# Performance work log

Hardware: AMD Instinct MI355X
Metric: run time of the kernel (lower is better)

## Reference

```python
import jax, jax.numpy as jnp
import numpy as np

B, N, D, H, DH, E, BIAS_DIM = 8, 512, 512, 8, 64, 32768, 8

def setup_inputs() -> dict:
    key = jax.random.key(0)
    ks = jax.random.split(key, 10)
    states = jax.random.normal(ks[0], (B, N, D), jnp.float32)
    key_states = jax.random.normal(ks[1], (B, N, D), jnp.float32)
    # causal mask, broadcastable over heads: [B,1,N,N]
    masks = jnp.broadcast_to(jnp.tril(jnp.ones((N, N), jnp.float32)), (B, 1, N, N))
    edge_type = jax.random.randint(ks[2], (E, 1), 0, BIAS_DIM, jnp.int32)
    b_idx = jax.random.randint(ks[3], (E, 1), 0, B, jnp.int32)
    q_idx = jax.random.randint(ks[4], (E, 1), 0, N, jnp.int32)
    k_idx = jax.random.randint(ks[5], (E, 1), 0, N, jnp.int32)
    attention_bias = jnp.concatenate([edge_type, b_idx, q_idx, k_idx], axis=1)
    s = 0.05
    Wq = jax.random.normal(ks[6], (D, H, DH), jnp.float32) * s
    Wk = jax.random.normal(ks[7], (D, H, DH), jnp.float32) * s
    Wv = jax.random.normal(ks[8], (D, H, DH), jnp.float32) * s
    k2 = jax.random.split(ks[9], 3)
    Wo = jax.random.normal(k2[0], (H, DH, D), jnp.float32) * s
    bias_embs = jax.random.normal(k2[1], (BIAS_DIM, DH), jnp.float32) * s
    bias_scalar = jax.random.normal(k2[2], (DH, 1), jnp.float32) * s
    return {"states": states, "key_states": key_states, "masks": masks,
            "attention_bias": attention_bias, "Wq": Wq, "Wk": Wk, "Wv": Wv,
            "Wo": Wo, "bias_embs": bias_embs, "bias_scalar": bias_scalar}

def reference(states, key_states, masks, attention_bias, Wq, Wk, Wv, Wo, bias_embs, bias_scalar):
    q = jnp.einsum('btd,dha->btha', states, Wq)
    k = jnp.einsum('btd,dha->btha', key_states, Wk)
    v = jnp.einsum('btd,dha->btha', key_states, Wv)
    alpha = jnp.einsum('bkha,bqha->bhqk', k, q)  # [B,H,Q,K]
    # sparse edge bias: embed edge types, project to scalar, scatter into [B,Q,K]
    et = attention_bias[:, 0]
    bias_vals = (bias_embs[et] @ bias_scalar)[:, 0]  # [E]
    bq, bk = alpha.shape[2], alpha.shape[3]
    bias_mat = jnp.zeros((alpha.shape[0], bq, bk), alpha.dtype)
    bias_mat = bias_mat.at[attention_bias[:, 1], attention_bias[:, 2], attention_bias[:, 3]].add(bias_vals)
    summed_keys = jnp.sum(k, axis=-1)  # [B,K,H]
    alpha = alpha + jnp.einsum('bqk,bkh->bhqk', bias_mat, summed_keys)
    alpha = alpha * jax.lax.rsqrt(jnp.float32(DH))
    neg = jnp.finfo(jnp.float32).min
    alpha = alpha * masks + (1.0 - jnp.ceil(masks)) * neg
    alpha = jax.nn.softmax(alpha, axis=-1)
    alpha = alpha * masks
    context = jnp.einsum('bhqk,bkha->bqha', alpha, v)
    return jnp.einsum('btha,had->btd', context, Wo)
```

## Files before the change

kernel.cpp:

```cpp
#include <hip/hip_runtime.h>

typedef unsigned short u16;
typedef unsigned int u32;
typedef __bf16 bf16x8 __attribute__((ext_vector_type(8)));
typedef float f32x4 __attribute__((ext_vector_type(4)));
typedef u16 u16x8 __attribute__((ext_vector_type(8)));
typedef u16 u16x4 __attribute__((ext_vector_type(4)));


__device__ __forceinline__ u16 f2b(float f) {
  union { float f; u32 i; } v; v.f = f;
  u32 r = v.i + 0x7fffu + ((v.i >> 16) & 1u);
  return (u16)(r >> 16);
}
__device__ __forceinline__ float b2f(u16 u) {
  union { u32 i; float f; } v; v.i = ((u32)u) << 16; return v.f;
}

__global__ void cvt_bf16(const float* __restrict__ s0, const float* __restrict__ s1,
                         u16* __restrict__ d0, u16* __restrict__ d1) {
  const float* src = blockIdx.y ? s1 : s0;
  u16* dst = blockIdx.y ? d1 : d0;
  int gid = blockIdx.x * 256 + threadIdx.x;
  const float4* sp = (const float4*)src + (size_t)gid * 2;
  float4 x0 = sp[0], x1 = sp[1];
  u16x8 p;
  p[0] = f2b(x0.x); p[1] = f2b(x0.y); p[2] = f2b(x0.z); p[3] = f2b(x0.w);
  p[4] = f2b(x1.x); p[5] = f2b(x1.y); p[6] = f2b(x1.z); p[7] = f2b(x1.w);
  *(u16x8*)(dst + (size_t)gid * 8) = p;
}

__global__ void transpose_w(const float* __restrict__ w0, const float* __restrict__ w1,
                            const float* __restrict__ w2, const float* __restrict__ w3,
                            u16* __restrict__ o0, u16* __restrict__ o1,
                            u16* __restrict__ o2, u16* __restrict__ o3) {
  __shared__ u16 t[32][33];
  const float* src; u16* dst; float sc = 1.f;
  if (blockIdx.z == 0)      { src = w0; dst = o0; sc = 0.125f; }
  else if (blockIdx.z == 1) { src = w1; dst = o1; }
  else if (blockIdx.z == 2) { src = w2; dst = o2; }
  else                      { src = w3; dst = o3; }
  int tx = threadIdx.x, ty = threadIdx.y;
  int c0 = blockIdx.x * 32, r0 = blockIdx.y * 32;
  #pragma unroll
  for (int i = ty; i < 32; i += 8) t[i][tx] = f2b(src[(r0 + i) * 512 + c0 + tx] * sc);
  __syncthreads();
  #pragma unroll
  for (int i = ty; i < 32; i += 8) dst[(c0 + i) * 512 + r0 + tx] = t[tx][i];
}

__global__ void scatter_bias(const int* __restrict__ ab, const float* __restrict__ be,
                             const float* __restrict__ bsc, float* __restrict__ bias_mat,
                             int n_edges) {
  __shared__ float tv[8];
  int tid = threadIdx.x;
  if (tid < 8) {
    float s = 0.f;
    #pragma unroll
    for (int a = 0; a < 64; a++) s += be[tid * 64 + a] * bsc[a];
    tv[tid] = s * 0.125f;
  }
  __syncthreads();
  int e = blockIdx.x * 256 + tid;
  if (e < n_edges) {
    int et = ab[e * 4 + 0];
    int b  = ab[e * 4 + 1];
    int qi = ab[e * 4 + 2];
    int ki = ab[e * 4 + 3];
    atomicAdd(&bias_mat[((size_t)b * 512 + qi) * 512 + ki], tv[et]);
  }
}

__global__ __launch_bounds__(256) void qkv_gemm(const u16* __restrict__ sb,
                                                const u16* __restrict__ kbin,
                                                const u16* __restrict__ wT,
                                                u16* __restrict__ qb,
                                                u16* __restrict__ kbo,
                                                u16* __restrict__ vtb) {
  __shared__ u16 As[128 * 72];
  __shared__ u16 Bs[128 * 72];
  int tid = threadIdx.x;
  int lane = tid & 63, wave = tid >> 6;
  int quad = lane >> 4, ln = lane & 15;
  int wr = wave >> 1, wc = wave & 1;
  int row0 = blockIdx.x * 128;
  int col0 = blockIdx.y * 128;
  const u16* A = (col0 < 512) ? sb : kbin;
  int ar = tid >> 1;
  int ac = (tid & 1) * 32;

  f32x4 acc[4][4];
  #pragma unroll
  for (int i = 0; i < 4; i++)
    #pragma unroll
    for (int j = 0; j < 4; j++) acc[i][j] = (f32x4){0.f, 0.f, 0.f, 0.f};

  const u16* ap = A + (size_t)(row0 + ar) * 512 + ac;
  const u16* bp = wT + (size_t)(col0 + ar) * 512 + ac;

  u16x8 ra0, ra1, ra2, ra3, rb0, rb1, rb2, rb3;
  ra0 = *(const u16x8*)(ap + 0);  ra1 = *(const u16x8*)(ap + 8);
  ra2 = *(const u16x8*)(ap + 16); ra3 = *(const u16x8*)(ap + 24);
  rb0 = *(const u16x8*)(bp + 0);  rb1 = *(const u16x8*)(bp + 8);
  rb2 = *(const u16x8*)(bp + 16); rb3 = *(const u16x8*)(bp + 24);

  for (int k0 = 0; k0 < 512; k0 += 64) {
    __syncthreads();
    *(u16x8*)&As[ar * 72 + ac + 0]  = ra0;  *(u16x8*)&As[ar * 72 + ac + 8]  = ra1;
    *(u16x8*)&As[ar * 72 + ac + 16] = ra2;  *(u16x8*)&As[ar * 72 + ac + 24] = ra3;
    *(u16x8*)&Bs[ar * 72 + ac + 0]  = rb0;  *(u16x8*)&Bs[ar * 72 + ac + 8]  = rb1;
    *(u16x8*)&Bs[ar * 72 + ac + 16] = rb2;  *(u16x8*)&Bs[ar * 72 + ac + 24] = rb3;
    __syncthreads();
    if (k0 < 448) {
      int kn = k0 + 64;
      ra0 = *(const u16x8*)(ap + kn + 0);  ra1 = *(const u16x8*)(ap + kn + 8);
      ra2 = *(const u16x8*)(ap + kn + 16); ra3 = *(const u16x8*)(ap + kn + 24);
      rb0 = *(const u16x8*)(bp + kn + 0);  rb1 = *(const u16x8*)(bp + kn + 8);
      rb2 = *(const u16x8*)(bp + kn + 16); rb3 = *(const u16x8*)(bp + kn + 24);
    }
    #pragma unroll
    for (int s = 0; s < 2; s++) {
      bf16x8 af[4], bfv[4];
      #pragma unroll
      for (int i = 0; i < 4; i++)
        af[i] = *(bf16x8*)&As[(wr * 64 + i * 16 + ln) * 72 + s * 32 + quad * 8];
      #pragma unroll
      for (int j = 0; j < 4; j++)
        bfv[j] = *(bf16x8*)&Bs[(wc * 64 + j * 16 + ln) * 72 + s * 32 + quad * 8];
      #pragma unroll
      for (int i = 0; i < 4; i++)
        #pragma unroll
        for (int j = 0; j < 4; j++)
          acc[i][j] = __builtin_amdgcn_mfma_f32_16x16x32_bf16(af[i], bfv[j], acc[i][j], 0, 0, 0);
    }
  }

  int region = col0 >> 9;
  int nbase = col0 & 511;
  if (region <= 1) {
    u16* Cout = region ? kbo : qb;
    #pragma unroll
    for (int i = 0; i < 4; i++)
      #pragma unroll
      for (int j = 0; j < 4; j++) {
        int mb = row0 + wr * 64 + i * 16 + quad * 4;
        int n = nbase + wc * 64 + j * 16 + ln;
        #pragma unroll
        for (int r = 0; r < 4; r++)
          Cout[(size_t)(mb + r) * 512 + n] = f2b(acc[i][j][r]);
      }
  } else {
    #pragma unroll
    for (int i = 0; i < 4; i++)
      #pragma unroll
      for (int j = 0; j < 4; j++) {
        int mb = row0 + wr * 64 + i * 16 + quad * 4;
        int bb = mb >> 9, t0 = mb & 511;
        int a_abs = nbase + wc * 64 + j * 16 + ln;
        int h = a_abs >> 6, a = a_abs & 63;
        u16x4 p;
        p[0] = f2b(acc[i][j][0]); p[1] = f2b(acc[i][j][1]);
        p[2] = f2b(acc[i][j][2]); p[3] = f2b(acc[i][j][3]);
        *(u16x4*)&vtb[(((size_t)bb * 8 + h) * 64 + a) * 512 + t0] = p;
      }
  }
}

__global__ __launch_bounds__(256) void out_gemm(const u16* __restrict__ A,
                                                const u16* __restrict__ BT,
                                                float* __restrict__ C) {
  __shared__ u16 As[128 * 72];
  __shared__ u16 Bs[128 * 72];
  int tid = threadIdx.x;
  int lane = tid & 63, wave = tid >> 6;
  int quad = lane >> 4, ln = lane & 15;
  int wr = wave >> 1, wc = wave & 1;
  int row0 = blockIdx.x * 128;
  int col0 = blockIdx.y * 128;
  int ar = tid >> 1;
  int ac = (tid & 1) * 32;

  f32x4 acc[4][4];
  #pragma unroll
  for (int i = 0; i < 4; i++)
    #pragma unroll
    for (int j = 0; j < 4; j++) acc[i][j] = (f32x4){0.f, 0.f, 0.f, 0.f};

  const u16* ap = A + (size_t)(row0 + ar) * 512 + ac;
  const u16* bp = BT + (size_t)(col0 + ar) * 512 + ac;

  u16x8 ra0, ra1, ra2, ra3, rb0, rb1, rb2, rb3;
  ra0 = *(const u16x8*)(ap + 0);  ra1 = *(const u16x8*)(ap + 8);
  ra2 = *(const u16x8*)(ap + 16); ra3 = *(const u16x8*)(ap + 24);
  rb0 = *(const u16x8*)(bp + 0);  rb1 = *(const u16x8*)(bp + 8);
  rb2 = *(const u16x8*)(bp + 16); rb3 = *(const u16x8*)(bp + 24);

  for (int k0 = 0; k0 < 512; k0 += 64) {
    __syncthreads();
    *(u16x8*)&As[ar * 72 + ac + 0]  = ra0;  *(u16x8*)&As[ar * 72 + ac + 8]  = ra1;
    *(u16x8*)&As[ar * 72 + ac + 16] = ra2;  *(u16x8*)&As[ar * 72 + ac + 24] = ra3;
    *(u16x8*)&Bs[ar * 72 + ac + 0]  = rb0;  *(u16x8*)&Bs[ar * 72 + ac + 8]  = rb1;
    *(u16x8*)&Bs[ar * 72 + ac + 16] = rb2;  *(u16x8*)&Bs[ar * 72 + ac + 24] = rb3;
    __syncthreads();
    if (k0 < 448) {
      int kn = k0 + 64;
      ra0 = *(const u16x8*)(ap + kn + 0);  ra1 = *(const u16x8*)(ap + kn + 8);
      ra2 = *(const u16x8*)(ap + kn + 16); ra3 = *(const u16x8*)(ap + kn + 24);
      rb0 = *(const u16x8*)(bp + kn + 0);  rb1 = *(const u16x8*)(bp + kn + 8);
      rb2 = *(const u16x8*)(bp + kn + 16); rb3 = *(const u16x8*)(bp + kn + 24);
    }
    #pragma unroll
    for (int s = 0; s < 2; s++) {
      bf16x8 af[4], bfv[4];
      #pragma unroll
      for (int i = 0; i < 4; i++)
        af[i] = *(bf16x8*)&As[(wr * 64 + i * 16 + ln) * 72 + s * 32 + quad * 8];
      #pragma unroll
      for (int j = 0; j < 4; j++)
        bfv[j] = *(bf16x8*)&Bs[(wc * 64 + j * 16 + ln) * 72 + s * 32 + quad * 8];
      #pragma unroll
      for (int i = 0; i < 4; i++)
        #pragma unroll
        for (int j = 0; j < 4; j++)
          acc[i][j] = __builtin_amdgcn_mfma_f32_16x16x32_bf16(af[i], bfv[j], acc[i][j], 0, 0, 0);
    }
  }
  #pragma unroll
  for (int i = 0; i < 4; i++)
    #pragma unroll
    for (int j = 0; j < 4; j++) {
      int mb = row0 + wr * 64 + i * 16 + quad * 4;
      int n = col0 + wc * 64 + j * 16 + ln;
      #pragma unroll
      for (int r = 0; r < 4; r++)
        C[(size_t)(mb + r) * 512 + n] = acc[i][j][r];
    }
}

__global__ void sumk2(const u16* __restrict__ k, float* __restrict__ summed) {
  int tri = blockIdx.x * 4 + (threadIdx.x >> 6);
  int lane = threadIdx.x & 63;
  int bh = tri >> 9, t = tri & 511;
  int b = bh >> 3, h = bh & 7;
  float x = b2f(k[((size_t)(b * 512 + t)) * 512 + h * 64 + lane]);
  #pragma unroll
  for (int o = 32; o; o >>= 1) x += __shfl_xor(x, o);
  if (lane == 0) summed[tri] = x;
}

__global__ __launch_bounds__(256) void attn_mfma(const u16* __restrict__ q,
                                                 const u16* __restrict__ k,
                                                 const u16* __restrict__ vt,
                                                 const float* __restrict__ bias_mat,
                                                 const float* __restrict__ summed,
                                                 u16* __restrict__ ctx) {
  __shared__ u16 Qs[64 * 72];
  __shared__ u16 Ks[64 * 72];
  __shared__ u16 Vt[64 * 72];
  __shared__ u16 Ps[4][16 * 72];
  int tid = threadIdx.x;
  int wave = tid >> 6, lane = tid & 63;
  int quad = lane >> 4, ln = lane & 15;
  int blk = blockIdx.x;
  int qt = blk & 7, bh = blk >> 3;
  int b = bh >> 3, h = bh & 7;
  int q0 = qt * 64;

  int sr = tid >> 2;
  int sc2 = (tid & 3) * 16;

  {
    const u16* qp = q + ((size_t)(b * 512 + q0 + sr)) * 512 + h * 64 + sc2;
    *(u16x8*)&Qs[sr * 72 + sc2] = *(const u16x8*)qp;
    *(u16x8*)&Qs[sr * 72 + sc2 + 8] = *(const u16x8*)(qp + 8);
  }

  float m_r[4], l_r[4];
  f32x4 o[4];
  #pragma unroll
  for (int r = 0; r < 4; r++) { m_r[r] = -3.40282347e38f; l_r[r] = 0.f; }
  #pragma unroll
  for (int nt = 0; nt < 4; nt++) o[nt] = (f32x4){0.f, 0.f, 0.f, 0.f};

  int last = qt;
  const u16* kp0 = k + ((size_t)(b * 512 + sr)) * 512 + h * 64 + sc2;
  const u16* vp0 = vt + ((size_t)(bh * 64 + sr)) * 512 + sc2;

  u16x8 rk0 = *(const u16x8*)kp0;
  u16x8 rk1 = *(const u16x8*)(kp0 + 8);
  u16x8 rv0 = *(const u16x8*)vp0;
  u16x8 rv1 = *(const u16x8*)(vp0 + 8);

  for (int kb = 0; kb <= last; kb++) {
    __syncthreads();
    *(u16x8*)&Ks[sr * 72 + sc2] = rk0;
    *(u16x8*)&Ks[sr * 72 + sc2 + 8] = rk1;
    *(u16x8*)&Vt[sr * 72 + sc2] = rv0;
    *(u16x8*)&Vt[sr * 72 + sc2 + 8] = rv1;
    __syncthreads();
    if (kb < last) {
      const u16* kp = kp0 + (size_t)(kb + 1) * 64 * 512;
      const u16* vp = vp0 + (kb + 1) * 64;
      rk0 = *(const u16x8*)kp;
      rk1 = *(const u16x8*)(kp + 8);
      rv0 = *(const u16x8*)vp;
      rv1 = *(const u16x8*)(vp + 8);
    }

    int qrow = q0 + wave * 16 + quad * 4;
    float skv[4], bias_r[4][4];
    #pragma unroll
    for (int nt = 0; nt < 4; nt++) {
      int t = kb * 64 + nt * 16 + ln;
      skv[nt] = summed[bh * 512 + t];
      const float* bp = bias_mat + ((size_t)(b * 512 + qrow)) * 512 + t;
      #pragma unroll
      for (int r = 0; r < 4; r++) bias_r[nt][r] = bp[(size_t)r * 512];
    }

    bf16x8 aq0 = *(bf16x8*)&Qs[(wave * 16 + ln) * 72 + quad * 8];
    bf16x8 aq1 = *(bf16x8*)&Qs[(wave * 16 + ln) * 72 + 32 + quad * 8];
    f32x4 s[4];
    #pragma unroll
    for (int nt = 0; nt < 4; nt++) {
      bf16x8 b0 = *(bf16x8*)&Ks[(nt * 16 + ln) * 72 + quad * 8];
      bf16x8 b1 = *(bf16x8*)&Ks[(nt * 16 + ln) * 72 + 32 + quad * 8];
      s[nt] = (f32x4){0.f, 0.f, 0.f, 0.f};
      s[nt] = __builtin_amdgcn_mfma_f32_16x16x32_bf16(aq0, b0, s[nt], 0, 0, 0);
      s[nt] = __builtin_amdgcn_mfma_f32_16x16x32_bf16(aq1, b1, s[nt], 0, 0, 0);
    }

    #pragma unroll
    for (int nt = 0; nt < 4; nt++) {
      int t = kb * 64 + nt * 16 + ln;
      #pragma unroll
      for (int r = 0; r < 4; r++) {
        float val = s[nt][r] + bias_r[nt][r] * skv[nt];
        s[nt][r] = (t <= qrow + r) ? val : -3.40282347e38f;
      }
    }

    float alpha[4];
    #pragma unroll
    for (int r = 0; r < 4; r++) {
      float tm = fmaxf(fmaxf(s[0][r], s[1][r]), fmaxf(s[2][r], s[3][r]));
      #pragma unroll
      for (int off = 8; off; off >>= 1) tm = fmaxf(tm, __shfl_xor(tm, off));
      float mn = fmaxf(m_r[r], tm);
      alpha[r] = __expf(m_r[r] - mn);
      m_r[r] = mn;
      float rs = 0.f;
      #pragma unroll
      for (int nt = 0; nt < 4; nt++) {
        float p = __expf(s[nt][r] - mn);
        s[nt][r] = p;
        rs += p;
      }
      #pragma unroll
      for (int off = 8; off; off >>= 1) rs += __shfl_xor(rs, off);
      l_r[r] = l_r[r] * alpha[r] + rs;
    }

    #pragma unroll
    for (int nt = 0; nt < 4; nt++)
      #pragma unroll
      for (int r = 0; r < 4; r++)
        Ps[wave][(quad * 4 + r) * 72 + nt * 16 + ln] = f2b(s[nt][r]);
    #pragma unroll
    for (int nt = 0; nt < 4; nt++)
      #pragma unroll
      for (int r = 0; r < 4; r++)
        o[nt][r] *= alpha[r];

    bf16x8 ap0 = *(bf16x8*)&Ps[wave][ln * 72 + quad * 8];
    bf16x8 ap1 = *(bf16x8*)&Ps[wave][ln * 72 + 32 + quad * 8];
    #pragma unroll
    for (int nt = 0; nt < 4; nt++) {
      bf16x8 b0 = *(bf16x8*)&Vt[(nt * 16 + ln) * 72 + quad * 8];
      bf16x8 b1 = *(bf16x8*)&Vt[(nt * 16 + ln) * 72 + 32 + quad * 8];
      o[nt] = __builtin_amdgcn_mfma_f32_16x16x32_bf16(ap0, b0, o[nt], 0, 0, 0);
      o[nt] = __builtin_amdgcn_mfma_f32_16x16x32_bf16(ap1, b1, o[nt], 0, 0, 0);
    }
  }

  #pragma unroll
  for (int r = 0; r < 4; r++) {
    float inv = 1.f / l_r[r];
    int qrow = q0 + wave * 16 + quad * 4 + r;
    u16* dst = ctx + ((size_t)(b * 512 + qrow)) * 512 + h * 64;
    #pragma unroll
    for (int nt = 0; nt < 4; nt++)
      dst[nt * 16 + ln] = f2b(o[nt][r] * inv);
  }
}

extern "C" void kernel_launch(void* const* d_in, const int* in_sizes, int n_in,
                              void* d_out, int out_size, void* d_ws, size_t ws_size,
                              hipStream_t stream) {
  const float* states     = (const float*)d_in[0];
  const float* key_states = (const float*)d_in[1];
  const int*   ab         = (const int*)d_in[3];
  const float* Wq         = (const float*)d_in[4];
  const float* Wk         = (const float*)d_in[5];
  const float* Wv         = (const float*)d_in[6];
  const float* Wo         = (const float*)d_in[7];
  const float* be         = (const float*)d_in[8];
  const float* bsc        = (const float*)d_in[9];
  float* out = (float*)d_out;

  char* ws = (char*)d_ws;
  const size_t MB = 1024 * 1024;
  u16* wqt      = (u16*)(ws);
  u16* wkt      = (u16*)(ws + 512 * 1024);
  u16* wvt      = (u16*)(ws + 1024 * 1024);
  u16* wot      = (u16*)(ws + 1536 * 1024);
  u16* sb       = (u16*)(ws + 2 * MB);
  u16* kbin     = (u16*)(ws + 6 * MB);
  u16* qb       = (u16*)(ws + 10 * MB);
  u16* kbo      = (u16*)(ws + 14 * MB);
  u16* vtb      = (u16*)(ws + 18 * MB);
  u16* ctxb     = (u16*)(ws + 22 * MB);
  float* bias_m = (float*)(ws + 26 * MB);
  float* summed = (float*)(ws + 34 * MB);

  int n_edges = in_sizes[3] / 4;

  hipMemsetAsync(bias_m, 0, (size_t)8 * MB, stream);
  cvt_bf16<<<dim3(1024, 2), 256, 0, stream>>>(states, key_states, sb, kbin);
  transpose_w<<<dim3(16, 16, 4), dim3(32, 8), 0, stream>>>(Wq, Wk, Wv, Wo, wqt, wkt, wvt, wot);
  scatter_bias<<<dim3((n_edges + 255) / 256), 256, 0, stream>>>(ab, be, bsc, bias_m, n_edges);
  qkv_gemm<<<dim3(32, 12), 256, 0, stream>>>(sb, kbin, wqt, qb, kbo, vtb);
  sumk2<<<dim3(8192), 256, 0, stream>>>(kbo, summed);
  attn_mfma<<<dim3(512), 256, 0, stream>>>(qb, kbo, vtb, bias_m, summed, ctxb);
  out_gemm<<<dim3(32, 4), 256, 0, stream>>>(ctxb, wot, out);
}
```

Measured before the change: 156.6 us.

## Fuse prologue kernels, vectorize key sum, and pair causal query tiles per block

Merges the bf16 conversion, weight transpose and bias scatter into one prologue launch. The key-sum kernel now has each thread load eight bf16 values and reduce over eight lanes, which cuts its grid from 8192 blocks to 1024. Each attention block now handles two query tiles (p and 7-p), so every block does the same amount of causal work, and the grid drops from 512 to 256 blocks. The intent is to cut launch overhead and the tail imbalance of causal attention, at the cost of fewer attention blocks in flight and serial work within each block.

```diff
diff --git a/kernel.cpp b/kernel.cpp
--- a/kernel.cpp
+++ b/kernel.cpp
@@ -17,57 +17,61 @@
   union { u32 i; float f; } v; v.i = ((u32)u) << 16; return v.f;
 }
 
-__global__ void cvt_bf16(const float* __restrict__ s0, const float* __restrict__ s1,
-                         u16* __restrict__ d0, u16* __restrict__ d1) {
-  const float* src = blockIdx.y ? s1 : s0;
-  u16* dst = blockIdx.y ? d1 : d0;
-  int gid = blockIdx.x * 256 + threadIdx.x;
-  const float4* sp = (const float4*)src + (size_t)gid * 2;
-  float4 x0 = sp[0], x1 = sp[1];
-  u16x8 p;
-  p[0] = f2b(x0.x); p[1] = f2b(x0.y); p[2] = f2b(x0.z); p[3] = f2b(x0.w);
-  p[4] = f2b(x1.x); p[5] = f2b(x1.y); p[6] = f2b(x1.z); p[7] = f2b(x1.w);
-  *(u16x8*)(dst + (size_t)gid * 8) = p;
-}
-
-__global__ void transpose_w(const float* __restrict__ w0, const float* __restrict__ w1,
-                            const float* __restrict__ w2, const float* __restrict__ w3,
-                            u16* __restrict__ o0, u16* __restrict__ o1,
-                            u16* __restrict__ o2, u16* __restrict__ o3) {
+__global__ __launch_bounds__(256) void prologue(
+    const float* __restrict__ states, const float* __restrict__ key_states,
+    const float* __restrict__ Wq, const float* __restrict__ Wk,
+    const float* __restrict__ Wv, const float* __restrict__ Wo,
+    const int* __restrict__ ab, const float* __restrict__ be,
+    const float* __restrict__ bsc,
+    u16* __restrict__ sb, u16* __restrict__ kbin, u16* __restrict__ wbase,
+    float* __restrict__ bias_mat, int n_edges) {
   __shared__ u16 t[32][33];
-  const float* src; u16* dst; float sc = 1.f;
-  if (blockIdx.z == 0)      { src = w0; dst = o0; sc = 0.125f; }
-  else if (blockIdx.z == 1) { src = w1; dst = o1; }
-  else if (blockIdx.z == 2) { src = w2; dst = o2; }
-  else                      { src = w3; dst = o3; }
-  int tx = threadIdx.x, ty = threadIdx.y;
-  int c0 = blockIdx.x * 32, r0 = blockIdx.y * 32;
-  #pragma unroll
-  for (int i = ty; i < 32; i += 8) t[i][tx] = f2b(src[(r0 + i) * 512 + c0 + tx] * sc);
-  __syncthreads();
-  #pragma unroll
-  for (int i = ty; i < 32; i += 8) dst[(c0 + i) * 512 + r0 + tx] = t[tx][i];
-}
-
-__global__ void scatter_bias(const int* __restrict__ ab, const float* __restrict__ be,
-                             const float* __restrict__ bsc, float* __restrict__ bias_mat,
-                             int n_edges) {
   __shared__ float tv[8];
+  int bid = blockIdx.x;
   int tid = threadIdx.x;
-  if (tid < 8) {
-    float s = 0.f;
-    #pragma unroll
-    for (int a = 0; a < 64; a++) s += be[tid * 64 + a] * bsc[a];
-    tv[tid] = s * 0.125f;
-  }
-  __syncthreads();
-  int e = blockIdx.x * 256 + tid;
-  if (e < n_edges) {
-    int et = ab[e * 4 + 0];
-    int b  = ab[e * 4 + 1];
-    int qi = ab[e * 4 + 2];
-    int ki = ab[e * 4 + 3];
-    atomicAdd(&bias_mat[((size_t)b * 512 + qi) * 512 + ki], tv[et]);
+  if (bid < 2048) {
+    const float* src = (bid >= 1024) ? key_states : states;
+    u16* dst = (bid >= 1024) ? kbin : sb;
+    int gid = (bid & 1023) * 256 + tid;
+    const float4* sp = (const float4*)src + (size_t)gid * 2;
+    float4 x0 = sp[0], x1 = sp[1];
+    u16x8 p;
+    p[0] = f2b(x0.x); p[1] = f2b(x0.y); p[2] = f2b(x0.z); p[3] = f2b(x0.w);
+    p[4] = f2b(x1.x); p[5] = f2b(x1.y); p[6] = f2b(x1.z); p[7] = f2b(x1.w);
+    *(u16x8*)(dst + (size_t)gid * 8) = p;
+  } else if (bid < 3072) {
+    int tt = bid - 2048;
+    int z = tt >> 8, rem = tt & 255;
+    int bx = rem & 15, by = rem >> 4;
+    const float* src; float sc = 1.f;
+    if (z == 0)      { src = Wq; sc = 0.125f; }
+    else if (z == 1) { src = Wk; }
+    else if (z == 2) { src = Wv; }
+    else             { src = Wo; }
+    u16* dst = wbase + (size_t)z * 262144;
+    int tx = tid & 31, ty = tid >> 5;
+    int c0 = bx * 32, r0 = by * 32;
+    #pragma unroll
+    for (int i = ty; i < 32; i += 8) t[i][tx] = f2b(src[(r0 + i) * 512 + c0 + tx] * sc);
+    __syncthreads();
+    #pragma unroll
+    for (int i = ty; i < 32; i += 8) dst[(c0 + i) * 512 + r0 + tx] = t[tx][i];
+  } else {
+    if (tid < 8) {
+      float s = 0.f;
+      #pragma unroll
+      for (int a = 0; a < 64; a++) s += be[tid * 64 + a] * bsc[a];
+      tv[tid] = s * 0.125f;
+    }
+    __syncthreads();
+    int e = (bid - 3072) * 256 + tid;
+    if (e < n_edges) {
+      int et = ab[e * 4 + 0];
+      int b  = ab[e * 4 + 1];
+      int qi = ab[e * 4 + 2];
+      int ki = ab[e * 4 + 3];
+      atomicAdd(&bias_mat[((size_t)b * 512 + qi) * 512 + ki], tv[et]);
+    }
   }
 }
 
@@ -237,15 +241,21 @@
     }
 }
 
-__global__ void sumk2(const u16* __restrict__ k, float* __restrict__ summed) {
-  int tri = blockIdx.x * 4 + (threadIdx.x >> 6);
-  int lane = threadIdx.x & 63;
-  int bh = tri >> 9, t = tri & 511;
-  int b = bh >> 3, h = bh & 7;
-  float x = b2f(k[((size_t)(b * 512 + t)) * 512 + h * 64 + lane]);
+__global__ __launch_bounds__(256) void sumk2(const u16* __restrict__ k,
+                                             float* __restrict__ summed) {
+  int gid = blockIdx.x * 256 + threadIdx.x;
+  int group = gid >> 3;
+  int b = group >> 12, rem = group & 4095;
+  int t = rem >> 3, h = rem & 7;
+  int j = gid & 7;
+  u16x8 x = *(const u16x8*)(k + ((size_t)(b * 512 + t)) * 512 + h * 64 + j * 8);
+  float s = 0.f;
   #pragma unroll
-  for (int o = 32; o; o >>= 1) x += __shfl_xor(x, o);
-  if (lane == 0) summed[tri] = x;
+  for (int e = 0; e < 8; e++) s += b2f(x[e]);
+  s += __shfl_xor(s, 1);
+  s += __shfl_xor(s, 2);
+  s += __shfl_xor(s, 4);
+  if (j == 0) summed[(b * 8 + h) * 512 + t] = s;
 }
 
 __global__ __launch_bounds__(256) void attn_mfma(const u16* __restrict__ q,
@@ -262,135 +272,140 @@
   int wave = tid >> 6, lane = tid & 63;
   int quad = lane >> 4, ln = lane & 15;
   int blk = blockIdx.x;
-  int qt = blk & 7, bh = blk >> 3;
+  int p = blk & 3, bh = blk >> 2;
   int b = bh >> 3, h = bh & 7;
-  int q0 = qt * 64;
 
   int sr = tid >> 2;
   int sc2 = (tid & 3) * 16;
 
-  {
-    const u16* qp = q + ((size_t)(b * 512 + q0 + sr)) * 512 + h * 64 + sc2;
-    *(u16x8*)&Qs[sr * 72 + sc2] = *(const u16x8*)qp;
-    *(u16x8*)&Qs[sr * 72 + sc2 + 8] = *(const u16x8*)(qp + 8);
-  }
-
-  float m_r[4], l_r[4];
-  f32x4 o[4];
-  #pragma unroll
-  for (int r = 0; r < 4; r++) { m_r[r] = -3.40282347e38f; l_r[r] = 0.f; }
-  #pragma unroll
-  for (int nt = 0; nt < 4; nt++) o[nt] = (f32x4){0.f, 0.f, 0.f, 0.f};
-
-  int last = qt;
   const u16* kp0 = k + ((size_t)(b * 512 + sr)) * 512 + h * 64 + sc2;
   const u16* vp0 = vt + ((size_t)(bh * 64 + sr)) * 512 + sc2;
 
-  u16x8 rk0 = *(const u16x8*)kp0;
-  u16x8 rk1 = *(const u16x8*)(kp0 + 8);
-  u16x8 rv0 = *(const u16x8*)vp0;
-  u16x8 rv1 = *(const u16x8*)(vp0 + 8);
-
-  for (int kb = 0; kb <= last; kb++) {
-    __syncthreads();
-    *(u16x8*)&Ks[sr * 72 + sc2] = rk0;
-    *(u16x8*)&Ks[sr * 72 + sc2 + 8] = rk1;
-    *(u16x8*)&Vt[sr * 72 + sc2] = rv0;
-    *(u16x8*)&Vt[sr * 72 + sc2 + 8] = rv1;
-    __syncthreads();
-    if (kb < last) {
-      const u16* kp = kp0 + (size_t)(kb + 1) * 64 * 512;
-      const u16* vp = vp0 + (kb + 1) * 64;
-      rk0 = *(const u16x8*)kp;
-      rk1 = *(const u16x8*)(kp + 8);
-      rv0 = *(const u16x8*)vp;
-      rv1 = *(const u16x8*)(vp + 8);
-    }
-
-    int qrow = q0 + wave * 16 + quad * 4;
-    float skv[4], bias_r[4][4];
-    #pragma unroll
-    for (int nt = 0; nt < 4; nt++) {
-      int t = kb * 64 + nt * 16 + ln;
-      skv[nt] = summed[bh * 512 + t];
-      const float* bp = bias_mat + ((size_t)(b * 512 + qrow)) * 512 + t;
-      #pragma unroll
-      for (int r = 0; r < 4; r++) bias_r[nt][r] = bp[(size_t)r * 512];
-    }
-
-    bf16x8 aq0 = *(bf16x8*)&Qs[(wave * 16 + ln) * 72 + quad * 8];
-    bf16x8 aq1 = *(bf16x8*)&Qs[(wave * 16 + ln) * 72 + 32 + quad * 8];
-    f32x4 s[4];
-    #pragma unroll
-    for (int nt = 0; nt < 4; nt++) {
-      bf16x8 b0 = *(bf16x8*)&Ks[(nt * 16 + ln) * 72 + quad * 8];
-      bf16x8 b1 = *(bf16x8*)&Ks[(nt * 16 + ln) * 72 + 32 + quad * 8];
-      s[nt] = (f32x4){0.f, 0.f, 0.f, 0.f};
-      s[nt] = __builtin_amdgcn_mfma_f32_16x16x32_bf16(aq0, b0, s[nt], 0, 0, 0);
-      s[nt] = __builtin_amdgcn_mfma_f32_16x16x32_bf16(aq1, b1, s[nt], 0, 0, 0);
-    }
-
-    #pragma unroll
-    for (int nt = 0; nt < 4; nt++) {
-      int t = kb * 64 + nt * 16 + ln;
+  #pragma unroll
+  for (int ph = 0; ph < 2; ph++) {
+    int qt = ph ? (7 - p) : p;
+    int q0 = qt * 64;
+
+    __syncthreads();
+    {
+      const u16* qp = q + ((size_t)(b * 512 + q0 + sr)) * 512 + h * 64 + sc2;
+      *(u16x8*)&Qs[sr * 72 + sc2] = *(const u16x8*)qp;
+      *(u16x8*)&Qs[sr * 72 + sc2 + 8] = *(const u16x8*)(qp + 8);
+    }
+
+    float m_r[4], l_r[4];
+    f32x4 o[4];
+    #pragma unroll
+    for (int r = 0; r < 4; r++) { m_r[r] = -3.40282347e38f; l_r[r] = 0.f; }
+    #pragma unroll
+    for (int nt = 0; nt < 4; nt++) o[nt] = (f32x4){0.f, 0.f, 0.f, 0.f};
+
+    u16x8 rk0 = *(const u16x8*)kp0;
+    u16x8 rk1 = *(const u16x8*)(kp0 + 8);
+    u16x8 rv0 = *(const u16x8*)vp0;
+    u16x8 rv1 = *(const u16x8*)(vp0 + 8);
+
+    for (int kb = 0; kb <= qt; kb++) {
+      __syncthreads();
+      *(u16x8*)&Ks[sr * 72 + sc2] = rk0;
+      *(u16x8*)&Ks[sr * 72 + sc2 + 8] = rk1;
+      *(u16x8*)&Vt[sr * 72 + sc2] = rv0;
+      *(u16x8*)&Vt[sr * 72 + sc2 + 8] = rv1;
+      __syncthreads();
+      if (kb < qt) {
+        const u16* kp = kp0 + (size_t)(kb + 1) * 64 * 512;
+        const u16* vp = vp0 + (kb + 1) * 64;
+        rk0 = *(const u16x8*)kp;
+        rk1 = *(const u16x8*)(kp + 8);
+        rv0 = *(const u16x8*)vp;
+        rv1 = *(const u16x8*)(vp + 8);
+      }
+
+      int qrow = q0 + wave * 16 + quad * 4;
+      float skv[4], bias_r[4][4];
+      #pragma unroll
+      for (int nt = 0; nt < 4; nt++) {
+        int t = kb * 64 + nt * 16 + ln;
+        skv[nt] = summed[bh * 512 + t];
+        const float* bp = bias_mat + ((size_t)(b * 512 + qrow)) * 512 + t;
+        #pragma unroll
+        for (int r = 0; r < 4; r++) bias_r[nt][r] = bp[(size_t)r * 512];
+      }
+
+      bf16x8 aq0 = *(bf16x8*)&Qs[(wave * 16 + ln) * 72 + quad * 8];
+      bf16x8 aq1 = *(bf16x8*)&Qs[(wave * 16 + ln) * 72 + 32 + quad * 8];
+      f32x4 s[4];
+      #pragma unroll
+      for (int nt = 0; nt < 4; nt++) {
+        bf16x8 b0 = *(bf16x8*)&Ks[(nt * 16 + ln) * 72 + quad * 8];
+        bf16x8 b1 = *(bf16x8*)&Ks[(nt * 16 + ln) * 72 + 32 + quad * 8];
+        s[nt] = (f32x4){0.f, 0.f, 0.f, 0.f};
+        s[nt] = __builtin_amdgcn_mfma_f32_16x16x32_bf16(aq0, b0, s[nt], 0, 0, 0);
+        s[nt] = __builtin_amdgcn_mfma_f32_16x16x32_bf16(aq1, b1, s[nt], 0, 0, 0);
+      }
+
+      #pragma unroll
+      for (int nt = 0; nt < 4; nt++) {
+        int t = kb * 64 + nt * 16 + ln;
+        #pragma unroll
+        for (int r = 0; r < 4; r++) {
+          float val = s[nt][r] + bias_r[nt][r] * skv[nt];
+          s[nt][r] = (t <= qrow + r) ? val : -3.40282347e38f;
+        }
+      }
+
+      float alpha[4];
       #pragma unroll
       for (int r = 0; r < 4; r++) {
-        float val = s[nt][r] + bias_r[nt][r] * skv[nt];
-        s[nt][r] = (t <= qrow + r) ? val : -3.40282347e38f;
-      }
-    }
-
-    float alpha[4];
+        float tm = fmaxf(fmaxf(s[0][r], s[1][r]), fmaxf(s[2][r], s[3][r]));
+        #pragma unroll
+        for (int off = 8; off; off >>= 1) tm = fmaxf(tm, __shfl_xor(tm, off));
+        float mn = fmaxf(m_r[r], tm);
+        alpha[r] = __expf(m_r[r] - mn);
+        m_r[r] = mn;
+        float rs = 0.f;
+        #pragma unroll
+        for (int nt = 0; nt < 4; nt++) {
+          float pp = __expf(s[nt][r] - mn);
+          s[nt][r] = pp;
+          rs += pp;
+        }
+        #pragma unroll
+        for (int off = 8; off; off >>= 1) rs += __shfl_xor(rs, off);
+        l_r[r] = l_r[r] * alpha[r] + rs;
+      }
+
+      #pragma unroll
+      for (int nt = 0; nt < 4; nt++)
+        #pragma unroll
+        for (int r = 0; r < 4; r++)
+          Ps[wave][(quad * 4 + r) * 72 + nt * 16 + ln] = f2b(s[nt][r]);
+      #pragma unroll
+      for (int nt = 0; nt < 4; nt++)
+        #pragma unroll
+        for (int r = 0; r < 4; r++)
+          o[nt][r] *= alpha[r];
+
+      bf16x8 ap0 = *(bf16x8*)&Ps[wave][ln * 72 + quad * 8];
+      bf16x8 ap1 = *(bf16x8*)&Ps[wave][ln * 72 + 32 + quad * 8];
+      #pragma unroll
+      for (int nt = 0; nt < 4; nt++) {
+        bf16x8 b0 = *(bf16x8*)&Vt[(nt * 16 + ln) * 72 + quad * 8];
+        bf16x8 b1 = *(bf16x8*)&Vt[(nt * 16 + ln) * 72 + 32 + quad * 8];
+        o[nt] = __builtin_amdgcn_mfma_f32_16x16x32_bf16(ap0, b0, o[nt], 0, 0, 0);
+        o[nt] = __builtin_amdgcn_mfma_f32_16x16x32_bf16(ap1, b1, o[nt], 0, 0, 0);
+      }
+    }
+
     #pragma unroll
     for (int r = 0; r < 4; r++) {
-      float tm = fmaxf(fmaxf(s[0][r], s[1][r]), fmaxf(s[2][r], s[3][r]));
-      #pragma unroll
-      for (int off = 8; off; off >>= 1) tm = fmaxf(tm, __shfl_xor(tm, off));
-      float mn = fmaxf(m_r[r], tm);
-      alpha[r] = __expf(m_r[r] - mn);
-      m_r[r] = mn;
-      float rs = 0.f;
-      #pragma unroll
-      for (int nt = 0; nt < 4; nt++) {
-        float p = __expf(s[nt][r] - mn);
-        s[nt][r] = p;
-        rs += p;
-      }
-      #pragma unroll
-      for (int off = 8; off; off >>= 1) rs += __shfl_xor(rs, off);
-      l_r[r] = l_r[r] * alpha[r] + rs;
-    }
-
-    #pragma unroll
-    for (int nt = 0; nt < 4; nt++)
-      #pragma unroll
-      for (int r = 0; r < 4; r++)
-        Ps[wave][(quad * 4 + r) * 72 + nt * 16 + ln] = f2b(s[nt][r]);
-    #pragma unroll
-    for (int nt = 0; nt < 4; nt++)
-      #pragma unroll
-      for (int r = 0; r < 4; r++)
-        o[nt][r] *= alpha[r];
-
-    bf16x8 ap0 = *(bf16x8*)&Ps[wave][ln * 72 + quad * 8];
-    bf16x8 ap1 = *(bf16x8*)&Ps[wave][ln * 72 + 32 + quad * 8];
-    #pragma unroll
-    for (int nt = 0; nt < 4; nt++) {
-      bf16x8 b0 = *(bf16x8*)&Vt[(nt * 16 + ln) * 72 + quad * 8];
-      bf16x8 b1 = *(bf16x8*)&Vt[(nt * 16 + ln) * 72 + 32 + quad * 8];
-      o[nt] = __builtin_amdgcn_mfma_f32_16x16x32_bf16(ap0, b0, o[nt], 0, 0, 0);
-      o[nt] = __builtin_amdgcn_mfma_f32_16x16x32_bf16(ap1, b1, o[nt], 0, 0, 0);
-    }
-  }
-
-  #pragma unroll
-  for (int r = 0; r < 4; r++) {
-    float inv = 1.f / l_r[r];
-    int qrow = q0 + wave * 16 + quad * 4 + r;
-    u16* dst = ctx + ((size_t)(b * 512 + qrow)) * 512 + h * 64;
-    #pragma unroll
-    for (int nt = 0; nt < 4; nt++)
-      dst[nt * 16 + ln] = f2b(o[nt][r] * inv);
+      float inv = 1.f / l_r[r];
+      int qrow = q0 + wave * 16 + quad * 4 + r;
+      u16* dst = ctx + ((size_t)(b * 512 + qrow)) * 512 + h * 64;
+      #pragma unroll
+      for (int nt = 0; nt < 4; nt++)
+        dst[nt * 16 + ln] = f2b(o[nt][r] * inv);
+    }
   }
 }
 
@@ -410,9 +425,7 @@
 
   char* ws = (char*)d_ws;
   const size_t MB = 1024 * 1024;
-  u16* wqt      = (u16*)(ws);
-  u16* wkt      = (u16*)(ws + 512 * 1024);
-  u16* wvt      = (u16*)(ws + 1024 * 1024);
+  u16* wbase    = (u16*)(ws);
   u16* wot      = (u16*)(ws + 1536 * 1024);
   u16* sb       = (u16*)(ws + 2 * MB);
   u16* kbin     = (u16*)(ws + 6 * MB);
@@ -426,11 +439,10 @@
   int n_edges = in_sizes[3] / 4;
 
   hipMemsetAsync(bias_m, 0, (size_t)8 * MB, stream);
-  cvt_bf16<<<dim3(1024, 2), 256, 0, stream>>>(states, key_states, sb, kbin);
-  transpose_w<<<dim3(16, 16, 4), dim3(32, 8), 0, stream>>>(Wq, Wk, Wv, Wo, wqt, wkt, wvt, wot);
-  scatter_bias<<<dim3((n_edges + 255) / 256), 256, 0, stream>>>(ab, be, bsc, bias_m, n_edges);
-  qkv_gemm<<<dim3(32, 12), 256, 0, stream>>>(sb, kbin, wqt, qb, kbo, vtb);
-  sumk2<<<dim3(8192), 256, 0, stream>>>(kbo, summed);
-  attn_mfma<<<dim3(512), 256, 0, stream>>>(qb, kbo, vtb, bias_m, summed, ctxb);
+  prologue<<<dim3(3072 + (n_edges + 255) / 256), 256, 0, stream>>>(
+      states, key_states, Wq, Wk, Wv, Wo, ab, be, bsc, sb, kbin, wbase, bias_m, n_edges);
+  qkv_gemm<<<dim3(32, 12), 256, 0, stream>>>(sb, kbin, wbase, qb, kbo, vtb);
+  sumk2<<<dim3(1024), 256, 0, stream>>>(kbo, summed);
+  attn_mfma<<<dim3(256), 256, 0, stream>>>(qb, kbo, vtb, bias_m, summed, ctxb);
   out_gemm<<<dim3(32, 4), 256, 0, stream>>>(ctxb, wot, out);
 }
```

After: 150.9 us. -3.6%, faster.
